# Performance work log

Hardware: AMD Instinct MI355X
Metric: run time of the kernel (lower is better)

Reference implementation:

```python
import jax, jax.numpy as jnp
import numpy as np

TOP_K = 5
TEMPERATURE = 0.1
EPS = 1e-12


def _normalize(x):
    # F.normalize(x, dim=-1): x / max(||x||, eps)
    n = jnp.linalg.norm(x, axis=-1, keepdims=True)
    return x / jnp.maximum(n, EPS)


def setup_inputs() -> dict:
    key = jax.random.key(0)
    k1, k2, k3 = jax.random.split(key, 3)
    B, N, D = 1024, 200000, 128
    query = jax.random.normal(k1, (B, D), dtype=jnp.float32)
    # memory bank stores L2-normalized keys (MemoryBank.build applies F.normalize)
    memory = _normalize(jax.random.normal(k2, (N, D), dtype=jnp.float32))
    index_map = jnp.arange(N, dtype=jnp.int64)
    exclude_indices = jax.random.randint(k3, (B,), 0, N, dtype=jnp.int64)
    return {"query": query, "memory": memory, "index_map": index_map,
            "exclude_indices": exclude_indices}


def reference(query, memory, index_map, exclude_indices):
    # cosine similarity: normalize query, memory is already normalized
    qn = _normalize(query)                       # [B, D]
    sim = qn @ memory.T                          # [B, N]
    # exclude own training sample (training-time self-exclusion)
    mask = exclude_indices[:, None] == index_map[None, :]   # [B, N]
    sim = jnp.where(mask, -jnp.inf, sim)
    # top-k (effective_top_k = min(top_k, N-1) = TOP_K here)
    top_sim, top_idx = jax.lax.top_k(sim, TOP_K)             # [B, K]
    weights = jax.nn.softmax(top_sim / TEMPERATURE, axis=-1)  # [B, K]
    vecs = memory[top_idx]                                   # [B, K, D]
    retrieved = jnp.einsum('bk,bkd->bd', weights, vecs)      # weighted sum
    retrieved = _normalize(retrieved)
    distances = 1.0 - top_sim[:, 0]                          # [B]
    return retrieved, distances, weights
```

## Files before the change

### kernel.cpp

```cpp
#include <hip/hip_runtime.h>
#include <math.h>

#define D128 128
#define TOPK 5
#define NP 200704
#define NCH2 12544
#define NSTRIP 392
#define MARGIN 0.008f
#define CAP 1024

typedef __attribute__((ext_vector_type(8))) short short8;
typedef __attribute__((ext_vector_type(4))) float f32x4;

__device__ __forceinline__ short f2bf(float f) {
    union { float f; unsigned u; } c; c.f = f;
    unsigned u = c.u + 0x7FFFu + ((c.u >> 16) & 1u);
    return (short)(u >> 16);
}

template <int NN>
__device__ __forceinline__ void insertg(float (&v)[NN], int (&x)[NN], float nv, int nj) {
    bool g[NN];
    #pragma unroll
    for (int i = 0; i < NN; ++i) g[i] = nv > v[i];
    #pragma unroll
    for (int i = NN - 1; i > 0; --i) {
        v[i] = g[i - 1] ? v[i - 1] : (g[i] ? nv : v[i]);
        x[i] = g[i - 1] ? x[i - 1] : (g[i] ? nj : x[i]);
    }
    v[0] = g[0] ? nv : v[0];
    x[0] = g[0] ? nj : x[0];
}
template <int NN>
__device__ __forceinline__ void insertv(float (&v)[NN], float nv) {
    bool g[NN];
    #pragma unroll
    for (int i = 0; i < NN; ++i) g[i] = nv > v[i];
    #pragma unroll
    for (int i = NN - 1; i > 0; --i)
        v[i] = g[i - 1] ? v[i - 1] : (g[i] ? nv : v[i]);
    v[0] = g[0] ? nv : v[0];
}

__global__ void qnorm_kernel(const float* __restrict__ q, float* __restrict__ qn,
                             short* __restrict__ qbf) {
    int b = blockIdx.x, t = threadIdx.x;
    float v0 = q[(size_t)b * D128 + t];
    float v1 = q[(size_t)b * D128 + t + 64];
    float ss = v0 * v0 + v1 * v1;
    #pragma unroll
    for (int off = 32; off > 0; off >>= 1) ss += __shfl_xor(ss, off, 64);
    float scale = 1.0f / fmaxf(sqrtf(ss), 1e-12f);
    float a0 = v0 * scale, a1 = v1 * scale;
    qn[(size_t)b * D128 + t] = a0;
    qn[(size_t)b * D128 + t + 64] = a1;
    qbf[(size_t)b * D128 + t] = f2bf(a0);
    qbf[(size_t)b * D128 + t + 64] = f2bf(a1);
}

__global__ void mconv_kernel(const float* __restrict__ mem, short* __restrict__ mbf, int N) {
    int idx = blockIdx.x * 256 + threadIdx.x;
    if (idx >= NP * 16) return;
    int row = idx >> 4, seg = idx & 15;
    short8 out;
    if (row < N) {
        const float* p = mem + (size_t)row * D128 + seg * 8;
        #pragma unroll
        for (int i = 0; i < 8; ++i) out[i] = f2bf(p[i]);
    } else {
        #pragma unroll
        for (int i = 0; i < 8; ++i) out[i] = 0;
    }
    *(short8*)(mbf + (size_t)row * D128 + seg * 8) = out;
}

#define MFMA16(a, b, c) __builtin_amdgcn_mfma_f32_16x16x32_bf16(a, b, c, 0, 0, 0)

__global__ __launch_bounds__(256, 3) void simtopk_max(
    const short* __restrict__ qbf, const short* __restrict__ mbf,
    _Float16* __restrict__ candT) {
    __shared__ short sK[64 * 136];
    __shared__ _Float16 sC[256 * 40];
    const int strip = blockIdx.x;
    const int qsg = blockIdx.y;
    const int t = threadIdx.x, w = t >> 6, lane = t & 63;
    const int n = lane & 15, quad = lane >> 4;
    const int qbase = qsg * 256 + w * 64;

    short8 bq[4][4];
    #pragma unroll
    for (int f = 0; f < 4; ++f) {
        const short* qrow = qbf + (size_t)(qbase + f * 16 + n) * D128 + quad * 8;
        #pragma unroll
        for (int s = 0; s < 4; ++s) bq[f][s] = *(const short8*)(qrow + s * 32);
    }

    const size_t k0 = (size_t)strip * 512;
    const int srow = t >> 4, scol = t & 15;
    const short* gbase = mbf + (k0 + srow) * D128 + scol * 8;

    short8 r0, r1, r2, r3;
    r0 = *(const short8*)(gbase + (size_t)0 * 16 * D128);
    r1 = *(const short8*)(gbase + (size_t)1 * 16 * D128);
    r2 = *(const short8*)(gbase + (size_t)2 * 16 * D128);
    r3 = *(const short8*)(gbase + (size_t)3 * 16 * D128);
    *(short8*)(&sK[(srow +  0) * 136 + scol * 8]) = r0;
    *(short8*)(&sK[(srow + 16) * 136 + scol * 8]) = r1;
    *(short8*)(&sK[(srow + 32) * 136 + scol * 8]) = r2;
    *(short8*)(&sK[(srow + 48) * 136 + scol * 8]) = r3;
    __syncthreads();
    {
        const short* g = gbase + (size_t)1 * 64 * D128;
        r0 = *(const short8*)(g + (size_t)0 * 16 * D128);
        r1 = *(const short8*)(g + (size_t)1 * 16 * D128);
        r2 = *(const short8*)(g + (size_t)2 * 16 * D128);
        r3 = *(const short8*)(g + (size_t)3 * 16 * D128);
    }

    for (int round = 0; round < 8; ++round) {
        #pragma unroll
        for (int tt = 0; tt < 4; ++tt) {
            const short* ab = &sK[(tt * 16 + n) * 136 + quad * 8];
            short8 a0 = *(const short8*)(ab);
            short8 a1 = *(const short8*)(ab + 32);
            short8 a2 = *(const short8*)(ab + 64);
            short8 a3 = *(const short8*)(ab + 96);
            f32x4 c0 = {0.f, 0.f, 0.f, 0.f}, c1 = c0, c2 = c0, c3 = c0;
            c0 = MFMA16(a0, bq[0][0], c0);
            c1 = MFMA16(a0, bq[1][0], c1);
            c2 = MFMA16(a0, bq[2][0], c2);
            c3 = MFMA16(a0, bq[3][0], c3);
            c0 = MFMA16(a1, bq[0][1], c0);
            c1 = MFMA16(a1, bq[1][1], c1);
            c2 = MFMA16(a1, bq[2][1], c2);
            c3 = MFMA16(a1, bq[3][1], c3);
            c0 = MFMA16(a2, bq[0][2], c0);
            c1 = MFMA16(a2, bq[1][2], c1);
            c2 = MFMA16(a2, bq[2][2], c2);
            c3 = MFMA16(a2, bq[3][2], c3);
            c0 = MFMA16(a3, bq[0][3], c0);
            c1 = MFMA16(a3, bq[1][3], c1);
            c2 = MFMA16(a3, bq[2][3], c2);
            c3 = MFMA16(a3, bq[3][3], c3);
            float m0 = fmaxf(fmaxf(c0[0], c0[1]), fmaxf(c0[2], c0[3]));
            float m1 = fmaxf(fmaxf(c1[0], c1[1]), fmaxf(c1[2], c1[3]));
            float m2 = fmaxf(fmaxf(c2[0], c2[1]), fmaxf(c2[2], c2[3]));
            float m3 = fmaxf(fmaxf(c3[0], c3[1]), fmaxf(c3[2], c3[3]));
            m0 = fmaxf(m0, __shfl_xor(m0, 16, 64)); m0 = fmaxf(m0, __shfl_xor(m0, 32, 64));
            m1 = fmaxf(m1, __shfl_xor(m1, 16, 64)); m1 = fmaxf(m1, __shfl_xor(m1, 32, 64));
            m2 = fmaxf(m2, __shfl_xor(m2, 16, 64)); m2 = fmaxf(m2, __shfl_xor(m2, 32, 64));
            m3 = fmaxf(m3, __shfl_xor(m3, 16, 64)); m3 = fmaxf(m3, __shfl_xor(m3, 32, 64));
            float msel = (quad == 0) ? m0 : (quad == 1) ? m1 : (quad == 2) ? m2 : m3;
            sC[(w * 64 + quad * 16 + n) * 40 + round * 4 + tt] = (_Float16)msel;
        }
        if (round < 7) {
            __syncthreads();
            *(short8*)(&sK[(srow +  0) * 136 + scol * 8]) = r0;
            *(short8*)(&sK[(srow + 16) * 136 + scol * 8]) = r1;
            *(short8*)(&sK[(srow + 32) * 136 + scol * 8]) = r2;
            *(short8*)(&sK[(srow + 48) * 136 + scol * 8]) = r3;
            __syncthreads();
            if (round < 6) {
                const short* g = gbase + (size_t)(round + 2) * 64 * D128;
                r0 = *(const short8*)(g + (size_t)0 * 16 * D128);
                r1 = *(const short8*)(g + (size_t)1 * 16 * D128);
                r2 = *(const short8*)(g + (size_t)2 * 16 * D128);
                r3 = *(const short8*)(g + (size_t)3 * 16 * D128);
            }
        }
    }

    __syncthreads();
    {
        int q = qsg * 256 + t;
        short* dst = (short*)candT + (size_t)q * NCH2 + strip * 32;
        #pragma unroll
        for (int j = 0; j < 4; ++j)
            *(short8*)(dst + j * 8) = *(const short8*)(&sC[t * 40 + j * 8]);
    }
}

__global__ __launch_bounds__(256, 4) void finalize_batch(
    const _Float16* __restrict__ candT, const float* __restrict__ mem,
    const float* __restrict__ qn, const int* __restrict__ index_map,
    const int* __restrict__ excl,
    float* __restrict__ outR, float* __restrict__ outD, float* __restrict__ outW, int N) {
    const int q = blockIdx.x, t = threadIdx.x;
    const int w = t >> 6, lane = t & 63;

    __shared__ _Float16 sM[NCH2];
    __shared__ float sQ[D128];
    __shared__ unsigned short sList[CAP];
    __shared__ int sCnt, sOv;
    __shared__ float sThr;
    __shared__ float sMrg[4 * 6];
    __shared__ float sWv[4 * TOPK];
    __shared__ int   sWk[4 * TOPK];
    __shared__ float sW[TOPK];
    __shared__ int   sJ[TOPK];

    if (t < 128) sQ[t] = qn[(size_t)q * D128 + t];
    if (t == 0) { sCnt = 0; sOv = 0; }
    {
        const short* crow = (const short*)candT + (size_t)q * NCH2;
        for (int i = t; i < NCH2 / 8; i += 256)
            *(short8*)(&sM[i * 8]) = *(const short8*)(crow + i * 8);
    }
    __syncthreads();

    float pv[6];
    #pragma unroll
    for (int i = 0; i < 6; ++i) pv[i] = -3e38f;
    for (int i = t; i < NCH2; i += 256) {
        float v = (float)sM[i];
        if (v > pv[5]) insertv<6>(pv, v);
    }
    #pragma unroll
    for (int r = 0; r < 6; ++r) {
        float bv = pv[0];
        #pragma unroll
        for (int off = 32; off > 0; off >>= 1) bv = fmaxf(bv, __shfl_xor(bv, off, 64));
        int ml = (pv[0] == bv) ? lane : 64;
        #pragma unroll
        for (int off = 32; off > 0; off >>= 1) ml = min(ml, __shfl_xor(ml, off, 64));
        if (lane == ml) {
            #pragma unroll
            for (int i = 0; i < 5; ++i) pv[i] = pv[i + 1];
            pv[5] = -3e38f;
        }
        if (lane == 0) sMrg[w * 6 + r] = bv;
    }
    __syncthreads();
    if (t == 0) {
        float b6[6];
        #pragma unroll
        for (int i = 0; i < 6; ++i) b6[i] = -3e38f;
        for (int j = 0; j < 24; ++j) {
            float v = sMrg[j];
            if (v > b6[5]) insertv<6>(b6, v);
        }
        sThr = b6[5] - 2.0f * MARGIN;
    }
    __syncthreads();

    const float thr = sThr;
    for (int i = t; i < NCH2; i += 256) {
        if ((float)sM[i] >= thr) {
            int p = atomicAdd(&sCnt, 1);
            if (p < CAP) sList[p] = (unsigned short)i; else sOv = 1;
        }
    }
    __syncthreads();
    const int ov = sOv;
    const int cnt = ov ? NCH2 : min(sCnt, CAP);

    const int exq = excl[q];
    float tv[TOPK]; int ti[TOPK];
    #pragma unroll
    for (int i = 0; i < TOPK; ++i) { tv[i] = -3e38f; ti[i] = -1; }
    const int rounds = (cnt + 15) >> 4;
    for (int r = 0; r < rounds; ++r) {
        int slot = r * 16 + (t >> 4);
        int ch = (slot < cnt) ? (ov ? slot : (int)sList[slot]) : -1;
        int key = ch * 16 + (t & 15);
        float v = -3e38f;
        if (ch >= 0 && key < N && index_map[key] != exq) {
            const float4* mr = (const float4*)(mem + (size_t)key * D128);
            const float4* qv = (const float4*)sQ;
            float acc = 0.f;
            #pragma unroll
            for (int d = 0; d < 32; ++d) {
                float4 a = mr[d], b = qv[d];
                acc += a.x * b.x + a.y * b.y + a.z * b.z + a.w * b.w;
            }
            v = acc;
        }
        if (v > tv[TOPK - 1]) insertg<TOPK>(tv, ti, v, key);
    }

    #pragma unroll
    for (int r = 0; r < TOPK; ++r) {
        float bv = tv[0]; int bk = ti[0];
        #pragma unroll
        for (int off = 32; off > 0; off >>= 1) {
            float ovv = __shfl_xor(bv, off, 64);
            int   okk = __shfl_xor(bk, off, 64);
            if (ovv > bv || (ovv == bv && (unsigned)okk < (unsigned)bk)) { bv = ovv; bk = okk; }
        }
        if (tv[0] == bv && ti[0] == bk) {
            #pragma unroll
            for (int i = 0; i < TOPK - 1; ++i) { tv[i] = tv[i + 1]; ti[i] = ti[i + 1]; }
            tv[TOPK - 1] = -3e38f; ti[TOPK - 1] = -1;
        }
        if (lane == 0) { sWv[w * TOPK + r] = bv; sWk[w * TOPK + r] = bk; }
    }
    __syncthreads();
    if (t == 0) {
        float bv[TOPK]; int bi[TOPK];
        #pragma unroll
        for (int i = 0; i < TOPK; ++i) { bv[i] = -3e38f; bi[i] = -1; }
        for (int j = 0; j < 4 * TOPK; ++j) {
            float v = sWv[j];
            if (v > bv[TOPK - 1]) insertg<TOPK>(bv, bi, v, sWk[j]);
        }
        float m = bv[0], ex[TOPK], sum = 0.f;
        #pragma unroll
        for (int k = 0; k < TOPK; ++k) { ex[k] = __expf((bv[k] - m) * 10.0f); sum += ex[k]; }
        float inv = 1.0f / sum;
        #pragma unroll
        for (int k = 0; k < TOPK; ++k) {
            float wk = ex[k] * inv;
            sW[k] = wk; sJ[k] = bi[k];
            outW[(size_t)q * TOPK + k] = wk;
        }
        outD[q] = 1.0f - bv[0];
    }
    __syncthreads();
    if (t < 64) {
        float r0 = 0.f, r1 = 0.f;
        #pragma unroll
        for (int k = 0; k < TOPK; ++k) {
            const float* mr = mem + (size_t)sJ[k] * D128;
            r0 += sW[k] * mr[t];
            r1 += sW[k] * mr[t + 64];
        }
        float ss = r0 * r0 + r1 * r1;
        #pragma unroll
        for (int off = 32; off > 0; off >>= 1) ss += __shfl_xor(ss, off, 64);
        float scale = 1.0f / fmaxf(sqrtf(ss), 1e-12f);
        outR[(size_t)q * D128 + t]      = r0 * scale;
        outR[(size_t)q * D128 + t + 64] = r1 * scale;
    }
}

extern "C" void kernel_launch(void* const* d_in, const int* in_sizes, int n_in,
                              void* d_out, int out_size, void* d_ws, size_t ws_size,
                              hipStream_t stream) {
    const float* query  = (const float*)d_in[0];
    const float* memory = (const float*)d_in[1];
    const int* index_map = (const int*)d_in[2];
    const int* excl      = (const int*)d_in[3];

    const int B = in_sizes[3];
    const int N = in_sizes[2];

    char* ws = (char*)d_ws;
    float*    qn    = (float*)(ws);
    short*    qbf   = (short*)(ws + 524288);
    short*    mbf   = (short*)(ws + 786432);
    _Float16* candT = (_Float16*)(ws + 52166656);

    float* outR = (float*)d_out;
    float* outD = outR + (size_t)B * D128;
    float* outW = outD + B;

    qnorm_kernel<<<B, 64, 0, stream>>>(query, qn, qbf);
    mconv_kernel<<<(NP * 16 + 255) / 256, 256, 0, stream>>>(memory, mbf, N);
    dim3 gridC(NSTRIP, 4);
    simtopk_max<<<gridC, 256, 0, stream>>>(qbf, mbf, candT);
    finalize_batch<<<B, 256, 0, stream>>>(candT, memory, qn, index_map, excl,
                                          outR, outD, outW, N);
}
```

Measured before the change: 283.2 us.

## Double queries per wave in sim kernel and stream candidates from global in finalize

Each wave in the similarity kernel now covers 128 queries instead of 64. Every memory tile loaded into shared memory is therefore reused across twice as many MFMAs, and the grid's query dimension is halved. The finalize kernel no longer stages the candidate row in shared memory. It reads half8 vectors straight from global memory twice, once to find the threshold and once to collect candidates. The threshold is also changed from the sixth-best block-wide value to the maximum of the per-wave sixth-best values, which is cheaper to compute but may let more candidates through. The costs are higher register pressure (launch bounds drop to 2 blocks per CU) and a second global read of the candidate row.

```diff
diff --git a/kernel.cpp b/kernel.cpp
--- a/kernel.cpp
+++ b/kernel.cpp
@@ -10,6 +10,7 @@
 #define CAP 1024
 
 typedef __attribute__((ext_vector_type(8))) short short8;
+typedef __attribute__((ext_vector_type(8))) _Float16 half8;
 typedef __attribute__((ext_vector_type(4))) float f32x4;
 
 __device__ __forceinline__ short f2bf(float f) {
@@ -76,21 +77,21 @@
 
 #define MFMA16(a, b, c) __builtin_amdgcn_mfma_f32_16x16x32_bf16(a, b, c, 0, 0, 0)
 
-__global__ __launch_bounds__(256, 3) void simtopk_max(
+__global__ __launch_bounds__(256, 2) void simtopk_max(
     const short* __restrict__ qbf, const short* __restrict__ mbf,
     _Float16* __restrict__ candT) {
     __shared__ short sK[64 * 136];
-    __shared__ _Float16 sC[256 * 40];
+    __shared__ _Float16 sC[512 * 40];
     const int strip = blockIdx.x;
     const int qsg = blockIdx.y;
     const int t = threadIdx.x, w = t >> 6, lane = t & 63;
     const int n = lane & 15, quad = lane >> 4;
-    const int qbase = qsg * 256 + w * 64;
-
-    short8 bq[4][4];
-    #pragma unroll
-    for (int f = 0; f < 4; ++f) {
-        const short* qrow = qbf + (size_t)(qbase + f * 16 + n) * D128 + quad * 8;
+    const int qwbase = qsg * 512 + w * 128;
+
+    short8 bq[8][4];
+    #pragma unroll
+    for (int f = 0; f < 8; ++f) {
+        const short* qrow = qbf + (size_t)(qwbase + f * 16 + n) * D128 + quad * 8;
         #pragma unroll
         for (int s = 0; s < 4; ++s) bq[f][s] = *(const short8*)(qrow + s * 32);
     }
@@ -125,33 +126,31 @@
             short8 a1 = *(const short8*)(ab + 32);
             short8 a2 = *(const short8*)(ab + 64);
             short8 a3 = *(const short8*)(ab + 96);
-            f32x4 c0 = {0.f, 0.f, 0.f, 0.f}, c1 = c0, c2 = c0, c3 = c0;
-            c0 = MFMA16(a0, bq[0][0], c0);
-            c1 = MFMA16(a0, bq[1][0], c1);
-            c2 = MFMA16(a0, bq[2][0], c2);
-            c3 = MFMA16(a0, bq[3][0], c3);
-            c0 = MFMA16(a1, bq[0][1], c0);
-            c1 = MFMA16(a1, bq[1][1], c1);
-            c2 = MFMA16(a1, bq[2][1], c2);
-            c3 = MFMA16(a1, bq[3][1], c3);
-            c0 = MFMA16(a2, bq[0][2], c0);
-            c1 = MFMA16(a2, bq[1][2], c1);
-            c2 = MFMA16(a2, bq[2][2], c2);
-            c3 = MFMA16(a2, bq[3][2], c3);
-            c0 = MFMA16(a3, bq[0][3], c0);
-            c1 = MFMA16(a3, bq[1][3], c1);
-            c2 = MFMA16(a3, bq[2][3], c2);
-            c3 = MFMA16(a3, bq[3][3], c3);
-            float m0 = fmaxf(fmaxf(c0[0], c0[1]), fmaxf(c0[2], c0[3]));
-            float m1 = fmaxf(fmaxf(c1[0], c1[1]), fmaxf(c1[2], c1[3]));
-            float m2 = fmaxf(fmaxf(c2[0], c2[1]), fmaxf(c2[2], c2[3]));
-            float m3 = fmaxf(fmaxf(c3[0], c3[1]), fmaxf(c3[2], c3[3]));
-            m0 = fmaxf(m0, __shfl_xor(m0, 16, 64)); m0 = fmaxf(m0, __shfl_xor(m0, 32, 64));
-            m1 = fmaxf(m1, __shfl_xor(m1, 16, 64)); m1 = fmaxf(m1, __shfl_xor(m1, 32, 64));
-            m2 = fmaxf(m2, __shfl_xor(m2, 16, 64)); m2 = fmaxf(m2, __shfl_xor(m2, 32, 64));
-            m3 = fmaxf(m3, __shfl_xor(m3, 16, 64)); m3 = fmaxf(m3, __shfl_xor(m3, 32, 64));
-            float msel = (quad == 0) ? m0 : (quad == 1) ? m1 : (quad == 2) ? m2 : m3;
-            sC[(w * 64 + quad * 16 + n) * 40 + round * 4 + tt] = (_Float16)msel;
+            f32x4 c[8];
+            #pragma unroll
+            for (int f = 0; f < 8; ++f) c[f] = (f32x4){0.f, 0.f, 0.f, 0.f};
+            #pragma unroll
+            for (int f = 0; f < 8; ++f) c[f] = MFMA16(a0, bq[f][0], c[f]);
+            #pragma unroll
+            for (int f = 0; f < 8; ++f) c[f] = MFMA16(a1, bq[f][1], c[f]);
+            #pragma unroll
+            for (int f = 0; f < 8; ++f) c[f] = MFMA16(a2, bq[f][2], c[f]);
+            #pragma unroll
+            for (int f = 0; f < 8; ++f) c[f] = MFMA16(a3, bq[f][3], c[f]);
+            float m[8];
+            #pragma unroll
+            for (int f = 0; f < 8; ++f) {
+                float v = fmaxf(fmaxf(c[f][0], c[f][1]), fmaxf(c[f][2], c[f][3]));
+                v = fmaxf(v, __shfl_xor(v, 16, 64));
+                v = fmaxf(v, __shfl_xor(v, 32, 64));
+                m[f] = v;
+            }
+            {
+                float ma = (quad == 0) ? m[0] : (quad == 1) ? m[1] : (quad == 2) ? m[2] : m[3];
+                float mb = (quad == 0) ? m[4] : (quad == 1) ? m[5] : (quad == 2) ? m[6] : m[7];
+                sC[(w * 128 + quad * 16 + n) * 40 + round * 4 + tt] = (_Float16)ma;
+                sC[(w * 128 + (quad + 4) * 16 + n) * 40 + round * 4 + tt] = (_Float16)mb;
+            }
         }
         if (round < 7) {
             __syncthreads();
@@ -171,16 +170,18 @@
     }
 
     __syncthreads();
-    {
-        int q = qsg * 256 + t;
+    #pragma unroll
+    for (int j = 0; j < 2; ++j) {
+        int lq = t + j * 256;
+        int q = qsg * 512 + lq;
         short* dst = (short*)candT + (size_t)q * NCH2 + strip * 32;
         #pragma unroll
-        for (int j = 0; j < 4; ++j)
-            *(short8*)(dst + j * 8) = *(const short8*)(&sC[t * 40 + j * 8]);
-    }
-}
-
-__global__ __launch_bounds__(256, 4) void finalize_batch(
+        for (int k = 0; k < 4; ++k)
+            *(short8*)(dst + k * 8) = *(const short8*)(&sC[lq * 40 + k * 8]);
+    }
+}
+
+__global__ __launch_bounds__(256, 8) void finalize_batch(
     const _Float16* __restrict__ candT, const float* __restrict__ mem,
     const float* __restrict__ qn, const int* __restrict__ index_map,
     const int* __restrict__ excl,
@@ -188,12 +189,10 @@
     const int q = blockIdx.x, t = threadIdx.x;
     const int w = t >> 6, lane = t & 63;
 
-    __shared__ _Float16 sM[NCH2];
     __shared__ float sQ[D128];
+    __shared__ float sThrW[4];
     __shared__ unsigned short sList[CAP];
     __shared__ int sCnt, sOv;
-    __shared__ float sThr;
-    __shared__ float sMrg[4 * 6];
     __shared__ float sWv[4 * TOPK];
     __shared__ int   sWk[4 * TOPK];
     __shared__ float sW[TOPK];
@@ -201,53 +200,50 @@
 
     if (t < 128) sQ[t] = qn[(size_t)q * D128 + t];
     if (t == 0) { sCnt = 0; sOv = 0; }
+    const half8* crow8 = (const half8*)(candT + (size_t)q * NCH2);
+
+    float pv[6];
+    #pragma unroll
+    for (int i = 0; i < 6; ++i) pv[i] = -3e38f;
+    for (int i = t; i < NCH2 / 8; i += 256) {
+        half8 v8 = crow8[i];
+        #pragma unroll
+        for (int j = 0; j < 8; ++j) {
+            float v = (float)v8[j];
+            if (v > pv[5]) insertv<6>(pv, v);
+        }
+    }
     {
-        const short* crow = (const short*)candT + (size_t)q * NCH2;
-        for (int i = t; i < NCH2 / 8; i += 256)
-            *(short8*)(&sM[i * 8]) = *(const short8*)(crow + i * 8);
-    }
-    __syncthreads();
-
-    float pv[6];
-    #pragma unroll
-    for (int i = 0; i < 6; ++i) pv[i] = -3e38f;
-    for (int i = t; i < NCH2; i += 256) {
-        float v = (float)sM[i];
-        if (v > pv[5]) insertv<6>(pv, v);
-    }
-    #pragma unroll
-    for (int r = 0; r < 6; ++r) {
-        float bv = pv[0];
-        #pragma unroll
-        for (int off = 32; off > 0; off >>= 1) bv = fmaxf(bv, __shfl_xor(bv, off, 64));
-        int ml = (pv[0] == bv) ? lane : 64;
-        #pragma unroll
-        for (int off = 32; off > 0; off >>= 1) ml = min(ml, __shfl_xor(ml, off, 64));
-        if (lane == ml) {
-            #pragma unroll
-            for (int i = 0; i < 5; ++i) pv[i] = pv[i + 1];
-            pv[5] = -3e38f;
-        }
-        if (lane == 0) sMrg[w * 6 + r] = bv;
-    }
-    __syncthreads();
-    if (t == 0) {
-        float b6[6];
-        #pragma unroll
-        for (int i = 0; i < 6; ++i) b6[i] = -3e38f;
-        for (int j = 0; j < 24; ++j) {
-            float v = sMrg[j];
-            if (v > b6[5]) insertv<6>(b6, v);
-        }
-        sThr = b6[5] - 2.0f * MARGIN;
-    }
-    __syncthreads();
-
-    const float thr = sThr;
-    for (int i = t; i < NCH2; i += 256) {
-        if ((float)sM[i] >= thr) {
-            int p = atomicAdd(&sCnt, 1);
-            if (p < CAP) sList[p] = (unsigned short)i; else sOv = 1;
+        float b6 = -3e38f;
+        #pragma unroll
+        for (int r = 0; r < 6; ++r) {
+            float bv = pv[0];
+            #pragma unroll
+            for (int off = 32; off > 0; off >>= 1) bv = fmaxf(bv, __shfl_xor(bv, off, 64));
+            int ml = (pv[0] == bv) ? lane : 64;
+            #pragma unroll
+            for (int off = 32; off > 0; off >>= 1) ml = min(ml, __shfl_xor(ml, off, 64));
+            if (lane == ml) {
+                #pragma unroll
+                for (int i = 0; i < 5; ++i) pv[i] = pv[i + 1];
+                pv[5] = -3e38f;
+            }
+            b6 = bv;
+        }
+        if (lane == 0) sThrW[w] = b6;
+    }
+    __syncthreads();
+    const float thr = fmaxf(fmaxf(sThrW[0], sThrW[1]), fmaxf(sThrW[2], sThrW[3]))
+                      - 2.0f * MARGIN;
+
+    for (int i = t; i < NCH2 / 8; i += 256) {
+        half8 v8 = crow8[i];
+        #pragma unroll
+        for (int j = 0; j < 8; ++j) {
+            if ((float)v8[j] >= thr) {
+                int p = atomicAdd(&sCnt, 1);
+                if (p < CAP) sList[p] = (unsigned short)(i * 8 + j); else sOv = 1;
+            }
         }
     }
     __syncthreads();
@@ -356,7 +352,7 @@
 
     qnorm_kernel<<<B, 64, 0, stream>>>(query, qn, qbf);
     mconv_kernel<<<(NP * 16 + 255) / 256, 256, 0, stream>>>(memory, mbf, N);
-    dim3 gridC(NSTRIP, 4);
+    dim3 gridC(NSTRIP, 2);
     simtopk_max<<<gridC, 256, 0, stream>>>(qbf, mbf, candT);
     finalize_batch<<<B, 256, 0, stream>>>(candT, memory, qn, index_map, excl,
                                           outR, outD, outW, N);
```

After: 373.4 us. 31.8% more time.

## Add per-strip max summary so finalize scans only promising strips

Applied to the files above, without the earlier changes.

The similarity kernel now also writes each query's maximum over each 32-chunk strip to a small strip-max array. Finalize first derives its threshold from these 392 strip maxima, then reads only the chunk candidates inside strips that pass the threshold, instead of loading and scanning the full 12544-entry candidate row into shared memory. The smaller shared-memory footprint also allows a higher launch-bounds occupancy, and the memory conversion now uses float4 loads. The cost is an extra reduction and scattered store in the similarity kernel's epilogue, plus a threshold that may be looser and admit somewhat more candidate chunks.

```diff
diff --git a/kernel.cpp b/kernel.cpp
--- a/kernel.cpp
+++ b/kernel.cpp
@@ -10,6 +10,7 @@
 #define CAP 1024
 
 typedef __attribute__((ext_vector_type(8))) short short8;
+typedef __attribute__((ext_vector_type(8))) _Float16 half8;
 typedef __attribute__((ext_vector_type(4))) float f32x4;
 
 __device__ __forceinline__ short f2bf(float f) {
@@ -64,9 +65,10 @@
     int row = idx >> 4, seg = idx & 15;
     short8 out;
     if (row < N) {
-        const float* p = mem + (size_t)row * D128 + seg * 8;
-        #pragma unroll
-        for (int i = 0; i < 8; ++i) out[i] = f2bf(p[i]);
+        const float4* p = (const float4*)(mem + (size_t)row * D128 + seg * 8);
+        float4 a = p[0], b = p[1];
+        out[0] = f2bf(a.x); out[1] = f2bf(a.y); out[2] = f2bf(a.z); out[3] = f2bf(a.w);
+        out[4] = f2bf(b.x); out[5] = f2bf(b.y); out[6] = f2bf(b.z); out[7] = f2bf(b.w);
     } else {
         #pragma unroll
         for (int i = 0; i < 8; ++i) out[i] = 0;
@@ -78,7 +80,7 @@
 
 __global__ __launch_bounds__(256, 3) void simtopk_max(
     const short* __restrict__ qbf, const short* __restrict__ mbf,
-    _Float16* __restrict__ candT) {
+    _Float16* __restrict__ candT, _Float16* __restrict__ candS) {
     __shared__ short sK[64 * 136];
     __shared__ _Float16 sC[256 * 40];
     const int strip = blockIdx.x;
@@ -174,47 +176,49 @@
     {
         int q = qsg * 256 + t;
         short* dst = (short*)candT + (size_t)q * NCH2 + strip * 32;
-        #pragma unroll
-        for (int j = 0; j < 4; ++j)
-            *(short8*)(dst + j * 8) = *(const short8*)(&sC[t * 40 + j * 8]);
-    }
-}
-
-__global__ __launch_bounds__(256, 4) void finalize_batch(
-    const _Float16* __restrict__ candT, const float* __restrict__ mem,
-    const float* __restrict__ qn, const int* __restrict__ index_map,
-    const int* __restrict__ excl,
+        float mx = -3e38f;
+        #pragma unroll
+        for (int j = 0; j < 4; ++j) {
+            half8 h = *(const half8*)(&sC[t * 40 + j * 8]);
+            *(short8*)(dst + j * 8) = *(const short8*)(&h);
+            #pragma unroll
+            for (int e = 0; e < 8; ++e) mx = fmaxf(mx, (float)h[e]);
+        }
+        candS[(size_t)strip * 1024 + q] = (_Float16)mx;
+    }
+}
+
+__global__ __launch_bounds__(256, 8) void finalize_batch(
+    const _Float16* __restrict__ candT, const _Float16* __restrict__ candS,
+    const float* __restrict__ mem, const float* __restrict__ qn,
+    const int* __restrict__ index_map, const int* __restrict__ excl,
     float* __restrict__ outR, float* __restrict__ outD, float* __restrict__ outW, int N) {
     const int q = blockIdx.x, t = threadIdx.x;
     const int w = t >> 6, lane = t & 63;
 
-    __shared__ _Float16 sM[NCH2];
     __shared__ float sQ[D128];
-    __shared__ unsigned short sList[CAP];
+    __shared__ float sMrg[4 * 6];
+    __shared__ float sThr;
+    __shared__ unsigned short sStr[NSTRIP];
+    __shared__ int sNs;
+    __shared__ unsigned short sChk[CAP];
     __shared__ int sCnt, sOv;
-    __shared__ float sThr;
-    __shared__ float sMrg[4 * 6];
     __shared__ float sWv[4 * TOPK];
     __shared__ int   sWk[4 * TOPK];
     __shared__ float sW[TOPK];
     __shared__ int   sJ[TOPK];
 
     if (t < 128) sQ[t] = qn[(size_t)q * D128 + t];
-    if (t == 0) { sCnt = 0; sOv = 0; }
-    {
-        const short* crow = (const short*)candT + (size_t)q * NCH2;
-        for (int i = t; i < NCH2 / 8; i += 256)
-            *(short8*)(&sM[i * 8]) = *(const short8*)(crow + i * 8);
-    }
-    __syncthreads();
+    if (t == 0) { sNs = 0; sCnt = 0; sOv = 0; }
+
+    float v0 = (t < NSTRIP) ? (float)candS[(size_t)t * 1024 + q] : -3e38f;
+    float v1 = (t + 256 < NSTRIP) ? (float)candS[(size_t)(t + 256) * 1024 + q] : -3e38f;
 
     float pv[6];
     #pragma unroll
     for (int i = 0; i < 6; ++i) pv[i] = -3e38f;
-    for (int i = t; i < NCH2; i += 256) {
-        float v = (float)sM[i];
-        if (v > pv[5]) insertv<6>(pv, v);
-    }
+    if (v0 > pv[5]) insertv<6>(pv, v0);
+    if (v1 > pv[5]) insertv<6>(pv, v1);
     #pragma unroll
     for (int r = 0; r < 6; ++r) {
         float bv = pv[0];
@@ -242,12 +246,22 @@
         sThr = b6[5] - 2.0f * MARGIN;
     }
     __syncthreads();
-
     const float thr = sThr;
-    for (int i = t; i < NCH2; i += 256) {
-        if ((float)sM[i] >= thr) {
-            int p = atomicAdd(&sCnt, 1);
-            if (p < CAP) sList[p] = (unsigned short)i; else sOv = 1;
+
+    if (t < NSTRIP && v0 >= thr) { int p = atomicAdd(&sNs, 1); sStr[p] = (unsigned short)t; }
+    if (t + 256 < NSTRIP && v1 >= thr) { int p = atomicAdd(&sNs, 1); sStr[p] = (unsigned short)(t + 256); }
+    __syncthreads();
+    const int ns = sNs;
+
+    const _Float16* crow = candT + (size_t)q * NCH2;
+    for (int base = 0; base < ns; base += 8) {
+        int gi = base + (t >> 5);
+        if (gi < ns) {
+            int ch = (int)sStr[gi] * 32 + (t & 31);
+            if ((float)crow[ch] >= thr) {
+                int p = atomicAdd(&sCnt, 1);
+                if (p < CAP) sChk[p] = (unsigned short)ch; else sOv = 1;
+            }
         }
     }
     __syncthreads();
@@ -261,7 +275,7 @@
     const int rounds = (cnt + 15) >> 4;
     for (int r = 0; r < rounds; ++r) {
         int slot = r * 16 + (t >> 4);
-        int ch = (slot < cnt) ? (ov ? slot : (int)sList[slot]) : -1;
+        int ch = (slot < cnt) ? (ov ? slot : (int)sChk[slot]) : -1;
         int key = ch * 16 + (t & 15);
         float v = -3e38f;
         if (ch >= 0 && key < N && index_map[key] != exq) {
@@ -349,6 +363,7 @@
     short*    qbf   = (short*)(ws + 524288);
     short*    mbf   = (short*)(ws + 786432);
     _Float16* candT = (_Float16*)(ws + 52166656);
+    _Float16* candS = (_Float16*)(ws + 77856768);
 
     float* outR = (float*)d_out;
     float* outD = outR + (size_t)B * D128;
@@ -357,7 +372,7 @@
     qnorm_kernel<<<B, 64, 0, stream>>>(query, qn, qbf);
     mconv_kernel<<<(NP * 16 + 255) / 256, 256, 0, stream>>>(memory, mbf, N);
     dim3 gridC(NSTRIP, 4);
-    simtopk_max<<<gridC, 256, 0, stream>>>(qbf, mbf, candT);
-    finalize_batch<<<B, 256, 0, stream>>>(candT, memory, qn, index_map, excl,
+    simtopk_max<<<gridC, 256, 0, stream>>>(qbf, mbf, candT, candS);
+    finalize_batch<<<B, 256, 0, stream>>>(candT, candS, memory, qn, index_map, excl,
                                           outR, outD, outW, N);
 }
```

Result: slower. 302.9 us (+6.9%).
